# Kernel tuning notes

Hardware: AMD Instinct MI355X
Metric: run time of the kernel (lower is better)

Reference implementation:

```python
import jax, jax.numpy as jnp
import numpy as np

B, T, D, H = 8192, 128, 16, 32
EPS = 1e-5  # BatchNorm1d default eps (eval mode, running stats)


def setup_inputs() -> dict:
    key = jax.random.key(0)
    ks = iter(jax.random.split(key, 64))

    def nrm(shape, s=0.1):
        return jax.random.normal(next(ks), shape, jnp.float32) * s

    inp = {}
    inp["S"] = nrm((B, T, D), 1.0)
    inp["g_S"] = nrm((B, T), 1.0)
    inp["times"] = jnp.linspace(0.0, 1.0, T, dtype=jnp.float32)
    inp["payoff_T"] = nrm((B,), 1.0)
    inp["delta_T"] = nrm((B, D), 1.0)
    # init_hidden: uniform(-0.1, 0.1), shape [num_layers=2, B, H]
    inp["h_price0"] = jax.random.uniform(next(ks), (2, B, H), jnp.float32, -0.1, 0.1)
    inp["h_delta0"] = jax.random.uniform(next(ks), (2, B, H), jnp.float32, -0.1, 0.1)
    # params for price net (prefix p_, out_dim=1) and delta net (prefix d_, out_dim=D)
    for pfx, out_dim in (("p", 1), ("d", D)):
        inp[pfx + "_Wih0"] = nrm((3 * H, 2 * D))
        inp[pfx + "_Whh0"] = nrm((3 * H, H))
        inp[pfx + "_bih0"] = nrm((3 * H,))
        inp[pfx + "_bhh0"] = nrm((3 * H,))
        inp[pfx + "_Wih1"] = nrm((3 * H, H))
        inp[pfx + "_Whh1"] = nrm((3 * H, H))
        inp[pfx + "_bih1"] = nrm((3 * H,))
        inp[pfx + "_bhh1"] = nrm((3 * H,))
        inp[pfx + "_embW"] = nrm((H, H))
        inp[pfx + "_embB"] = nrm((H,))
        inp[pfx + "_bng"] = jnp.ones((H,), jnp.float32)
        inp[pfx + "_bnb"] = jnp.zeros((H,), jnp.float32)
        inp[pfx + "_bnm"] = nrm((H,))
        inp[pfx + "_bnv"] = jax.random.uniform(next(ks), (H,), jnp.float32, 0.5, 1.5)
        inp[pfx + "_outW"] = nrm((out_dim, H))
        inp[pfx + "_outB"] = nrm((out_dim,))
    return inp


def _gru_cell(x, h, Wih, Whh, bih, bhh):
    # PyTorch GRU cell, gate order (r, z, n)
    gi = x @ Wih.T + bih
    gh = h @ Whh.T + bhh
    ir, iz, inn = jnp.split(gi, 3, axis=-1)
    hr, hz, hn = jnp.split(gh, 3, axis=-1)
    r = jax.nn.sigmoid(ir + hr)
    z = jax.nn.sigmoid(iz + hz)
    n = jnp.tanh(inn + r * hn)
    return (1.0 - z) * n + z * h


def _head(y, Wemb, bemb, g, b, m, v, Wout, bout, sig):
    # Linear -> BatchNorm1d (eval, running stats) -> SiLU -> Linear [-> Sigmoid]
    e = y @ Wemb.T + bemb
    e = (e - m) * jax.lax.rsqrt(v + EPS) * g + b
    e = e * jax.nn.sigmoid(e)  # SiLU
    o = e @ Wout.T + bout
    return jax.nn.sigmoid(o) if sig else o


def reference(S, g_S, times, payoff_T, delta_T, h_price0, h_delta0,
              p_Wih0, p_Whh0, p_bih0, p_bhh0, p_Wih1, p_Whh1, p_bih1, p_bhh1,
              p_embW, p_embB, p_bng, p_bnb, p_bnm, p_bnv, p_outW, p_outB,
              d_Wih0, d_Whh0, d_bih0, d_bhh0, d_Wih1, d_Whh1, d_bih1, d_bhh1,
              d_embW, d_embB, d_bng, d_bnb, d_bnm, d_bnv, d_outW, d_outB):
    # X = cat([S, g_S expanded to d]) -> [B, T, 2D]
    gS = jnp.broadcast_to(g_S[..., None], S.shape)
    X = jnp.concatenate([S, gS], axis=-1)
    Xr = jnp.swapaxes(X, 0, 1)[::-1]  # [T, B, 2D], time reversed (loop goes t=T-1..0)

    def step(carry, xt):
        hp0, hp1, hd0, hd1 = carry
        hp0 = _gru_cell(xt, hp0, p_Wih0, p_Whh0, p_bih0, p_bhh0)
        hp1 = _gru_cell(hp0, hp1, p_Wih1, p_Whh1, p_bih1, p_bhh1)
        hd0 = _gru_cell(xt, hd0, d_Wih0, d_Whh0, d_bih0, d_bhh0)
        hd1 = _gru_cell(hd0, hd1, d_Wih1, d_Whh1, d_bih1, d_bhh1)
        return (hp0, hp1, hd0, hd1), (hp1, hd1)

    carry0 = (h_price0[0], h_price0[1], h_delta0[0], h_delta0[1])
    _, (Yp, Yd) = jax.lax.scan(step, carry0, Xr)
    # flip time back to forward order: outputs were collected for t=T-1..0
    Yp = jnp.swapaxes(Yp[::-1], 0, 1)  # [B, T, H]
    Yd = jnp.swapaxes(Yd[::-1], 0, 1)  # [B, T, H]
    prices = _head(Yp, p_embW, p_embB, p_bng, p_bnb, p_bnm, p_bnv, p_outW, p_outB, False)  # [B,T,1]
    deltas = _head(Yd, d_embW, d_embB, d_bng, d_bnb, d_bnm, d_bnv, d_outW, d_outB, True)   # [B,T,D]
    return (prices, deltas)
```

## Files before the change

### kernel.cpp

```cpp
#include <hip/hip_runtime.h>
#include <hip/hip_bf16.h>
#include <stdint.h>

#define DI __device__ __forceinline__

typedef float f32x4 __attribute__((ext_vector_type(4)));
typedef float f32x2 __attribute__((ext_vector_type(2)));
typedef short bf16x8 __attribute__((ext_vector_type(8)));

constexpr int BB = 8192, TT = 128, DD = 16, HH = 32;
constexpr float kEPS = 1e-5f;
constexpr float kLOG2E = 1.44269504088896340736f;

DI float rcpf_(float x) { return __builtin_amdgcn_rcpf(x); }
DI float exp2f_(float x) { return __builtin_amdgcn_exp2f(x); }
DI float sigm(float x) { return rcpf_(1.0f + exp2f_(-kLOG2E * x)); }

DI uint32_t cvtpk(float lo, float hi) {
  uint32_t r;
  asm("v_cvt_pk_bf16_f32 %0, %1, %2" : "=v"(r) : "v"(lo), "v"(hi));
  return r;
}

DI f32x4 mfma_(bf16x8 a, bf16x8 b, f32x4 c) {
  return __builtin_amdgcn_mfma_f32_16x16x32_bf16(a, b, c, 0, 0, 0);
}

union U4 { uint4 q; bf16x8 v; uint32_t u[4]; };

__global__ void prep_net(const float* Wih0, const float* Whh0,
                         const float* bih0, const float* bhh0,
                         const float* Wih1, const float* Whh1,
                         const float* bih1, const float* bhh1,
                         const float* embW, const float* embB,
                         const float* bng, const float* bnb,
                         const float* bnm, const float* bnv,
                         const float* outW, const float* outB,
                         int outDim, uint8_t* wsbase) {
  int tid = threadIdx.x;
  uint16_t* W = (uint16_t*)wsbase;
  float* bias = (float*)(wsbase + 27648);
  auto cvt = [](float f) -> uint16_t {
    union { float f; uint32_t u; } v; v.f = f;
    uint32_t u = v.u;
    return (uint16_t)((u + 0x7FFF + ((u >> 16) & 1)) >> 16);
  };
  const float oscale = (outDim == 16) ? -kLOG2E : 1.0f;
  for (int idx = tid; idx < 27 * 64; idx += 256) {
    int tile = idx >> 6, l = idx & 63, cc = l & 15, gg = l >> 4;
    uint16_t* dst = W + (size_t)idx * 8;
    if (tile < 24) {
      const float* mats[4] = {Wih0, Whh0, Wih1, Whh1};
      const float* src = mats[tile / 6];
      int sub = tile % 6;
      int row = sub * 16 + cc;
      float sc = (sub < 4) ? -kLOG2E : 2.0f * kLOG2E;
#pragma unroll
      for (int j = 0; j < 8; ++j) {
        int k = (j < 4) ? 4 * gg + j : 16 + 4 * gg + (j - 4);
        dst[j] = cvt(src[row * 32 + k] * sc);
      }
    } else if (tile < 26) {
      int row = (tile - 24) * 16 + cc;
      float a = bng[row] * rsqrtf(bnv[row] + kEPS);
#pragma unroll
      for (int j = 0; j < 8; ++j) {
        int k = (j < 4) ? 4 * gg + j : 16 + 4 * gg + (j - 4);
        dst[j] = cvt(embW[row * 32 + k] * a);
      }
    } else {
      int rrow = (cc < outDim) ? cc : 0;
      float sc = (cc < outDim) ? oscale : 0.0f;
#pragma unroll
      for (int j = 0; j < 8; ++j) {
        int k = (j < 4) ? 4 * gg + j : 16 + 4 * gg + (j - 4);
        dst[j] = cvt(outW[rrow * 32 + k] * sc);
      }
    }
  }
  for (int idx = tid; idx < 304; idx += 256) {
    int tile = idx >> 4, n = idx & 15;
    float v;
    if (tile < 8) {
      if (tile < 4)      v = (bih0[tile * 16 + n] + bhh0[tile * 16 + n]) * (-kLOG2E);
      else if (tile < 6) v = bih0[64 + (tile - 4) * 16 + n] * (2.0f * kLOG2E);
      else               v = bhh0[64 + (tile - 6) * 16 + n] * (2.0f * kLOG2E);
    } else if (tile < 16) {
      int tt = tile - 8;
      if (tt < 4)        v = (bih1[tt * 16 + n] + bhh1[tt * 16 + n]) * (-kLOG2E);
      else if (tt < 6)   v = bih1[64 + (tt - 4) * 16 + n] * (2.0f * kLOG2E);
      else               v = bhh1[64 + (tt - 6) * 16 + n] * (2.0f * kLOG2E);
    } else if (tile < 18) {
      int nn = (tile - 16) * 16 + n;
      float a = bng[nn] * rsqrtf(bnv[nn] + kEPS);
      v = a * (embB[nn] - bnm[nn]) + bnb[nn];
    } else {
      v = (n < outDim) ? outB[n] * oscale : 0.0f;
    }
    bias[idx] = v;
  }
}

__global__ __launch_bounds__(64, 1) void rnn_fused(
    const float* __restrict__ S, const float* __restrict__ gS,
    const float* __restrict__ hp0, const float* __restrict__ hd0,
    const uint8_t* __restrict__ ws, float* __restrict__ out) {
  const int lane = threadIdx.x & 63;
  const int net = blockIdx.x & 1;
  const int b0 = (blockIdx.x >> 1) * 16;
  const int c = lane & 15, g = lane >> 4;

  const uint16_t* W = (const uint16_t*)(ws + net * 32768);
  const float* bias = (const float*)(ws + net * 32768 + 27648);
  const float* hsrc = net ? hd0 : hp0;

  bf16x8 Wt[27];
#pragma unroll
  for (int t = 0; t < 27; ++t)
    Wt[t] = *(const bf16x8*)(W + (t * 64 + lane) * 8);
  f32x4 Bq[19];
#pragma unroll
  for (int t = 0; t < 19; ++t)
    Bq[t] = *(const f32x4*)(bias + t * 16 + 4 * g);

  auto packB = [&](const float (&v)[8]) -> bf16x8 {
    U4 t;
    t.u[0] = cvtpk(v[0], v[1]); t.u[1] = cvtpk(v[2], v[3]);
    t.u[2] = cvtpk(v[4], v[5]); t.u[3] = cvtpk(v[6], v[7]);
    return t.v;
  };

  auto gruStep = [&](int wih, int whh, int bb, bf16x8 xf, bf16x8 hf,
                     float (&hC)[8]) {
    f32x4 r0 = mfma_(Wt[wih + 0], xf, Bq[bb + 0]); r0 = mfma_(Wt[whh + 0], hf, r0);
    f32x4 r1 = mfma_(Wt[wih + 1], xf, Bq[bb + 1]); r1 = mfma_(Wt[whh + 1], hf, r1);
    f32x4 z0 = mfma_(Wt[wih + 2], xf, Bq[bb + 2]); z0 = mfma_(Wt[whh + 2], hf, z0);
    f32x4 z1 = mfma_(Wt[wih + 3], xf, Bq[bb + 3]); z1 = mfma_(Wt[whh + 3], hf, z1);
    f32x4 ni0 = mfma_(Wt[wih + 4], xf, Bq[bb + 4]);
    f32x4 ni1 = mfma_(Wt[wih + 5], xf, Bq[bb + 5]);
    f32x4 nh0 = mfma_(Wt[whh + 4], hf, Bq[bb + 6]);
    f32x4 nh1 = mfma_(Wt[whh + 5], hf, Bq[bb + 7]);
    const f32x2 one = {1.0f, 1.0f};
#pragma unroll
    for (int r = 0; r < 4; ++r) {
      f32x2 ra = {r0[r], r1[r]};
      f32x2 za = {z0[r], z1[r]};
      f32x2 ni = {ni0[r], ni1[r]};
      f32x2 nh = {nh0[r], nh1[r]};
      f32x2 hv = {hC[r], hC[4 + r]};
      f32x2 era = {exp2f_(ra[0]), exp2f_(ra[1])};
      f32x2 t1 = one + era;
      f32x2 rg = {rcpf_(t1[0]), rcpf_(t1[1])};
      f32x2 w = ni + rg * nh;
      f32x2 En = {exp2f_(w[0]), exp2f_(w[1])};
      f32x2 Ez = {exp2f_(za[0]), exp2f_(za[1])};
      f32x2 num = (hv - Ez) + En * (hv + Ez);
      f32x2 den = (one + En) * (one + Ez);
      f32x2 rd = {rcpf_(den[0]), rcpf_(den[1])};
      f32x2 res = num * rd;
      hC[r] = res[0]; hC[4 + r] = res[1];
    }
  };

  auto loadState = [&](const float* row, float (&hC)[8]) -> bf16x8 {
    f32x4 a = *(const f32x4*)(row + 4 * g);
    f32x4 b = *(const f32x4*)(row + 16 + 4 * g);
#pragma unroll
    for (int r = 0; r < 4; ++r) { hC[r] = a[r]; hC[4 + r] = b[r]; }
    U4 t;
    t.u[0] = cvtpk(a[0], a[1]); t.u[1] = cvtpk(a[2], a[3]);
    t.u[2] = cvtpk(b[0], b[1]); t.u[3] = cvtpk(b[2], b[3]);
    return t.v;
  };

  auto mkX = [&](f32x4 sv, float gsv) -> bf16x8 {
    uint32_t pkg = cvtpk(gsv, gsv);
    U4 t;
    t.u[0] = cvtpk(sv[0], sv[1]);
    t.u[1] = cvtpk(sv[2], sv[3]);
    t.u[2] = pkg;
    t.u[3] = pkg;
    return t.v;
  };

  auto head = [&](bf16x8 h1f, int th) {
    f32x4 e0 = mfma_(Wt[24], h1f, Bq[16]);
    f32x4 e1 = mfma_(Wt[25], h1f, Bq[17]);
    float es[8];
#pragma unroll
    for (int r = 0; r < 4; ++r) {
      float a = e0[r], b = e1[r];
      es[r]     = a * sigm(a);
      es[4 + r] = b * sigm(b);
    }
    bf16x8 ef = packB(es);
    f32x4 o = mfma_(Wt[26], ef, Bq[18]);
    if (net == 0) {
      if (lane < 16) out[(size_t)(b0 + c) * TT + th] = o[0];
    } else {
      f32x4 so;
#pragma unroll
      for (int r = 0; r < 4; ++r) so[r] = rcpf_(1.0f + exp2f_(o[r]));
      *(f32x4*)(out + (size_t)BB * TT +
                ((size_t)(b0 + c) * TT + th) * DD + 4 * g) = so;
    }
  };

  float h0C[8], h1C[8];
  bf16x8 h0B = loadState(hsrc + (size_t)(b0 + c) * HH, h0C);
  bf16x8 h1B = loadState(hsrc + ((size_t)BB + b0 + c) * HH, h1C);

  const float* Sbase  = S  + (size_t)(b0 + c) * TT * DD + 4 * g;
  const float* gSbase = gS + (size_t)(b0 + c) * TT;

  f32x4 xa = *(const f32x4*)(Sbase + (size_t)(TT - 1) * DD);
  float ga = gSbase[TT - 1];
  f32x4 xb = *(const f32x4*)(Sbase + (size_t)(TT - 2) * DD);
  float gb = gSbase[TT - 2];

  bf16x8 xB = mkX(xa, ga);
  gruStep(0, 6, 0, xB, h0B, h0C);
  h0B = packB(h0C);

#pragma unroll 1
  for (int t = TT - 2; t >= 0; --t) {
    xB = mkX(xb, gb);
    int tn = (t > 0) ? t - 1 : 0;
    xa = *(const f32x4*)(Sbase + (size_t)tn * DD);
    ga = gSbase[tn];

    gruStep(12, 18, 8, h0B, h1B, h1C);
    gruStep(0, 6, 0, xB, h0B, h0C);
    h1B = packB(h1C);
    h0B = packB(h0C);
    head(h1B, t + 1);

    xb = xa; gb = ga;
  }
  gruStep(12, 18, 8, h0B, h1B, h1C);
  h1B = packB(h1C);
  head(h1B, 0);
}

extern "C" void kernel_launch(void* const* d_in, const int* in_sizes, int n_in,
                              void* d_out, int out_size, void* d_ws,
                              size_t ws_size, hipStream_t stream) {
  const float* S   = (const float*)d_in[0];
  const float* gS  = (const float*)d_in[1];
  const float* hp0 = (const float*)d_in[5];
  const float* hd0 = (const float*)d_in[6];
  uint8_t* ws = (uint8_t*)d_ws;

  prep_net<<<1, 256, 0, stream>>>(
      (const float*)d_in[7],  (const float*)d_in[8],  (const float*)d_in[9],
      (const float*)d_in[10], (const float*)d_in[11], (const float*)d_in[12],
      (const float*)d_in[13], (const float*)d_in[14], (const float*)d_in[15],
      (const float*)d_in[16], (const float*)d_in[17], (const float*)d_in[18],
      (const float*)d_in[19], (const float*)d_in[20], (const float*)d_in[21],
      (const float*)d_in[22], 1, ws);
  prep_net<<<1, 256, 0, stream>>>(
      (const float*)d_in[23], (const float*)d_in[24], (const float*)d_in[25],
      (const float*)d_in[26], (const float*)d_in[27], (const float*)d_in[28],
      (const float*)d_in[29], (const float*)d_in[30], (const float*)d_in[31],
      (const float*)d_in[32], (const float*)d_in[33], (const float*)d_in[34],
      (const float*)d_in[35], (const float*)d_in[36], (const float*)d_in[37],
      (const float*)d_in[38], 16, ws + 32768);

  rnn_fused<<<dim3((BB / 16) * 2), dim3(64), 0, stream>>>(S, gS, hp0, hd0,
                                                          ws, (float*)d_out);
}
```

Baseline: 158.9 us.

## Software-pipeline GRU layers and head across timesteps with grouped MFMA issue

Splits the GRU step into an MFMA phase and a gate phase, then skews the output head so its embedding and output MFMAs run one and two steps behind the recurrence. Each iteration issues all MFMAs for layer 1, the head and layer 0 together, then does the elementwise gate, SiLU and store work, with sched_barriers keeping the two phases apart. The input prefetch is deepened to two steps ahead. The aim is to hide MFMA latency and the serial head dependency behind independent work, at the cost of more live registers and a longer prologue and epilogue.

```diff
diff --git a/kernel.cpp b/kernel.cpp
--- a/kernel.cpp
+++ b/kernel.cpp
@@ -130,23 +130,26 @@
     return t.v;
   };
 
-  auto gruStep = [&](int wih, int whh, int bb, bf16x8 xf, bf16x8 hf,
-                     float (&hC)[8]) {
-    f32x4 r0 = mfma_(Wt[wih + 0], xf, Bq[bb + 0]); r0 = mfma_(Wt[whh + 0], hf, r0);
-    f32x4 r1 = mfma_(Wt[wih + 1], xf, Bq[bb + 1]); r1 = mfma_(Wt[whh + 1], hf, r1);
-    f32x4 z0 = mfma_(Wt[wih + 2], xf, Bq[bb + 2]); z0 = mfma_(Wt[whh + 2], hf, z0);
-    f32x4 z1 = mfma_(Wt[wih + 3], xf, Bq[bb + 3]); z1 = mfma_(Wt[whh + 3], hf, z1);
-    f32x4 ni0 = mfma_(Wt[wih + 4], xf, Bq[bb + 4]);
-    f32x4 ni1 = mfma_(Wt[wih + 5], xf, Bq[bb + 5]);
-    f32x4 nh0 = mfma_(Wt[whh + 4], hf, Bq[bb + 6]);
-    f32x4 nh1 = mfma_(Wt[whh + 5], hf, Bq[bb + 7]);
+  auto mfmaGRU = [&](int wih, int whh, int bb, bf16x8 xf, bf16x8 hf,
+                     f32x4 (&A)[8]) {
+    A[0] = mfma_(Wt[wih + 0], xf, Bq[bb + 0]); A[0] = mfma_(Wt[whh + 0], hf, A[0]);
+    A[1] = mfma_(Wt[wih + 1], xf, Bq[bb + 1]); A[1] = mfma_(Wt[whh + 1], hf, A[1]);
+    A[2] = mfma_(Wt[wih + 2], xf, Bq[bb + 2]); A[2] = mfma_(Wt[whh + 2], hf, A[2]);
+    A[3] = mfma_(Wt[wih + 3], xf, Bq[bb + 3]); A[3] = mfma_(Wt[whh + 3], hf, A[3]);
+    A[4] = mfma_(Wt[wih + 4], xf, Bq[bb + 4]);
+    A[5] = mfma_(Wt[wih + 5], xf, Bq[bb + 5]);
+    A[6] = mfma_(Wt[whh + 4], hf, Bq[bb + 6]);
+    A[7] = mfma_(Wt[whh + 5], hf, Bq[bb + 7]);
+  };
+
+  auto gates = [&](const f32x4 (&A)[8], float (&hC)[8]) {
     const f32x2 one = {1.0f, 1.0f};
 #pragma unroll
     for (int r = 0; r < 4; ++r) {
-      f32x2 ra = {r0[r], r1[r]};
-      f32x2 za = {z0[r], z1[r]};
-      f32x2 ni = {ni0[r], ni1[r]};
-      f32x2 nh = {nh0[r], nh1[r]};
+      f32x2 ra = {A[0][r], A[1][r]};
+      f32x2 za = {A[2][r], A[3][r]};
+      f32x2 ni = {A[4][r], A[5][r]};
+      f32x2 nh = {A[6][r], A[7][r]};
       f32x2 hv = {hC[r], hC[4 + r]};
       f32x2 era = {exp2f_(ra[0]), exp2f_(ra[1])};
       f32x2 t1 = one + era;
@@ -162,6 +165,27 @@
     }
   };
 
+  auto silu = [&](const f32x4& e0, const f32x4& e1, float (&es)[8]) {
+#pragma unroll
+    for (int r = 0; r < 4; ++r) {
+      float a = e0[r], b = e1[r];
+      es[r]     = a * sigm(a);
+      es[4 + r] = b * sigm(b);
+    }
+  };
+
+  auto storeO = [&](const f32x4& o, int th) {
+    if (net == 0) {
+      if (lane < 16) out[(size_t)(b0 + c) * TT + th] = o[0];
+    } else {
+      f32x4 so;
+#pragma unroll
+      for (int r = 0; r < 4; ++r) so[r] = rcpf_(1.0f + exp2f_(o[r]));
+      *(f32x4*)(out + (size_t)BB * TT +
+                ((size_t)(b0 + c) * TT + th) * DD + 4 * g) = so;
+    }
+  };
+
   auto loadState = [&](const float* row, float (&hC)[8]) -> bf16x8 {
     f32x4 a = *(const f32x4*)(row + 4 * g);
     f32x4 b = *(const f32x4*)(row + 16 + 4 * g);
@@ -183,63 +207,82 @@
     return t.v;
   };
 
-  auto head = [&](bf16x8 h1f, int th) {
-    f32x4 e0 = mfma_(Wt[24], h1f, Bq[16]);
-    f32x4 e1 = mfma_(Wt[25], h1f, Bq[17]);
-    float es[8];
-#pragma unroll
-    for (int r = 0; r < 4; ++r) {
-      float a = e0[r], b = e1[r];
-      es[r]     = a * sigm(a);
-      es[4 + r] = b * sigm(b);
-    }
-    bf16x8 ef = packB(es);
-    f32x4 o = mfma_(Wt[26], ef, Bq[18]);
-    if (net == 0) {
-      if (lane < 16) out[(size_t)(b0 + c) * TT + th] = o[0];
-    } else {
-      f32x4 so;
-#pragma unroll
-      for (int r = 0; r < 4; ++r) so[r] = rcpf_(1.0f + exp2f_(o[r]));
-      *(f32x4*)(out + (size_t)BB * TT +
-                ((size_t)(b0 + c) * TT + th) * DD + 4 * g) = so;
-    }
-  };
-
-  float h0C[8], h1C[8];
+  const float* Sbase  = S  + (size_t)(b0 + c) * TT * DD + 4 * g;
+  const float* gSbase = gS + (size_t)(b0 + c) * TT;
+
+  float h0C[8], h1C[8], es[8];
   bf16x8 h0B = loadState(hsrc + (size_t)(b0 + c) * HH, h0C);
   bf16x8 h1B = loadState(hsrc + ((size_t)BB + b0 + c) * HH, h1C);
-
-  const float* Sbase  = S  + (size_t)(b0 + c) * TT * DD + 4 * g;
-  const float* gSbase = gS + (size_t)(b0 + c) * TT;
-
-  f32x4 xa = *(const f32x4*)(Sbase + (size_t)(TT - 1) * DD);
-  float ga = gSbase[TT - 1];
-  f32x4 xb = *(const f32x4*)(Sbase + (size_t)(TT - 2) * DD);
-  float gb = gSbase[TT - 2];
-
-  bf16x8 xB = mkX(xa, ga);
-  gruStep(0, 6, 0, xB, h0B, h0C);
+  bf16x8 ef, xB;
+  f32x4 A0[8], A1[8], e0, e1, o;
+
+  f32x4 xr0, xr1;
+  float gr0, gr1;
+  xB  = mkX(*(const f32x4*)(Sbase + (size_t)(TT - 1) * DD), gSbase[TT - 1]);
+  xr0 = *(const f32x4*)(Sbase + (size_t)(TT - 2) * DD); gr0 = gSbase[TT - 2];
+  xr1 = *(const f32x4*)(Sbase + (size_t)(TT - 3) * DD); gr1 = gSbase[TT - 3];
+  auto rollX = [&](int tn) {
+    xB = mkX(xr0, gr0);
+    xr0 = xr1; gr0 = gr1;
+    if (tn < 0) tn = 0;
+    xr1 = *(const f32x4*)(Sbase + (size_t)tn * DD); gr1 = gSbase[tn];
+  };
+
+  mfmaGRU(0, 6, 0, xB, h0B, A0);
+  gates(A0, h0C);
   h0B = packB(h0C);
+  rollX(TT - 4);
+  mfmaGRU(12, 18, 8, h0B, h1B, A1);
+  mfmaGRU(0, 6, 0, xB, h0B, A0);
+  gates(A1, h1C);
+  gates(A0, h0C);
+  h1B = packB(h1C); h0B = packB(h0C);
+  rollX(TT - 5);
+  mfmaGRU(12, 18, 8, h0B, h1B, A1);
+  e0 = mfma_(Wt[24], h1B, Bq[16]);
+  e1 = mfma_(Wt[25], h1B, Bq[17]);
+  mfmaGRU(0, 6, 0, xB, h0B, A0);
+  gates(A1, h1C);
+  gates(A0, h0C);
+  silu(e0, e1, es);
+  h1B = packB(h1C); h0B = packB(h0C); ef = packB(es);
+  rollX(TT - 6);
 
 #pragma unroll 1
-  for (int t = TT - 2; t >= 0; --t) {
-    xB = mkX(xb, gb);
-    int tn = (t > 0) ? t - 1 : 0;
-    xa = *(const f32x4*)(Sbase + (size_t)tn * DD);
-    ga = gSbase[tn];
-
-    gruStep(12, 18, 8, h0B, h1B, h1C);
-    gruStep(0, 6, 0, xB, h0B, h0C);
+  for (int t = TT - 4; t >= 0; --t) {
+    mfmaGRU(12, 18, 8, h0B, h1B, A1);
+    e0 = mfma_(Wt[24], h1B, Bq[16]);
+    e1 = mfma_(Wt[25], h1B, Bq[17]);
+    o  = mfma_(Wt[26], ef, Bq[18]);
+    mfmaGRU(0, 6, 0, xB, h0B, A0);
+    __builtin_amdgcn_sched_barrier(0);
+    gates(A1, h1C);
+    gates(A0, h0C);
+    silu(e0, e1, es);
+    storeO(o, t + 3);
+    __builtin_amdgcn_sched_barrier(0);
     h1B = packB(h1C);
     h0B = packB(h0C);
-    head(h1B, t + 1);
-
-    xb = xa; gb = ga;
+    ef  = packB(es);
+    rollX(t - 3);
   }
-  gruStep(12, 18, 8, h0B, h1B, h1C);
-  h1B = packB(h1C);
-  head(h1B, 0);
+
+  mfmaGRU(12, 18, 8, h0B, h1B, A1);
+  e0 = mfma_(Wt[24], h1B, Bq[16]);
+  e1 = mfma_(Wt[25], h1B, Bq[17]);
+  o  = mfma_(Wt[26], ef, Bq[18]);
+  gates(A1, h1C);
+  silu(e0, e1, es);
+  storeO(o, 2);
+  h1B = packB(h1C); ef = packB(es);
+  e0 = mfma_(Wt[24], h1B, Bq[16]);
+  e1 = mfma_(Wt[25], h1B, Bq[17]);
+  o  = mfma_(Wt[26], ef, Bq[18]);
+  silu(e0, e1, es);
+  storeO(o, 1);
+  ef = packB(es);
+  o = mfma_(Wt[26], ef, Bq[18]);
+  storeO(o, 0);
 }
 
 extern "C" void kernel_launch(void* const* d_in, const int* in_sizes, int n_in,
```

Result: faster. 147.5 us (-7.1%).
